# Kernel tuning notes

Hardware: AMD Instinct MI355X
Metric: run time of the kernel (lower is better)

The kernel has to match this reference:

```python
import jax, jax.numpy as jnp
import numpy as np

B = 2048      # number of binary mixtures
NPM = 30      # atoms per molecule
N = B * NPM   # total nodes per side
EPM = 120     # directed edges per molecule
IN_DIM = 74
H = 128
NC = 2


def setup_inputs() -> dict:
    key = jax.random.key(0)
    ks = jax.random.split(key, 24)
    rng = np.random.default_rng(0)
    off = np.repeat(np.arange(B, dtype=np.int64) * NPM, EPM)
    mk_idx = lambda: jnp.asarray((rng.integers(0, NPM, B * EPM) + off).astype(np.int32))

    def lin(k, fi, fo):
        return (jax.random.normal(k, (fi, fo), jnp.float32) / np.sqrt(fi)).astype(jnp.float32)

    inp = {
        'h1': jax.random.normal(ks[0], (N, IN_DIM), jnp.float32),
        'h2': jax.random.normal(ks[1], (N, IN_DIM), jnp.float32),
        'solv1_x': jax.random.uniform(ks[2], (B,), jnp.float32),
        'inter_hb': jax.random.uniform(ks[3], (B,), jnp.float32),
        'intra_hb1': jax.random.uniform(ks[4], (B,), jnp.float32),
        'intra_hb2': jax.random.uniform(ks[5], (B,), jnp.float32),
        'Wg1': lin(ks[6], IN_DIM, H), 'bg1': jnp.zeros((H,), jnp.float32),
        'Wg2': lin(ks[7], H, H), 'bg2': jnp.zeros((H,), jnp.float32),
        'Wp': lin(ks[8], H, H), 'bp': jnp.zeros((H,), jnp.float32),
        'We1': lin(ks[9], 1, 32), 'be1': jnp.zeros((32,), jnp.float32),
        'We2': lin(ks[10], 32, H * H), 'be2': jnp.zeros((H * H,), jnp.float32),
        'bnn': jnp.zeros((H,), jnp.float32),
        'Wih': lin(ks[11], H, 3 * H), 'bih': jnp.zeros((3 * H,), jnp.float32),
        'Whh': lin(ks[12], H, 3 * H), 'bhh': jnp.zeros((3 * H,), jnp.float32),
        'Wcl1': lin(ks[13], 2 * H, H), 'bcl1': jnp.zeros((H,), jnp.float32),
        'Wcl2': lin(ks[14], H, H), 'bcl2': jnp.zeros((H,), jnp.float32),
        'Wcl3': lin(ks[15], H, NC), 'bcl3': jnp.zeros((NC,), jnp.float32),
        'src1': mk_idx(), 'dst1': mk_idx(), 'src2': mk_idx(), 'dst2': mk_idx(),
    }
    return inp


def _graphconv(x, src, dst, W, b, n):
    # DGL GraphConv, norm='both': D_in^{-1/2} A D_out^{-1/2} X W + b
    ones = jnp.ones(src.shape[0], x.dtype)
    d_out = jnp.maximum(jax.ops.segment_sum(ones, src, num_segments=n), 1.0)
    d_in = jnp.maximum(jax.ops.segment_sum(ones, dst, num_segments=n), 1.0)
    m = (x * jax.lax.rsqrt(d_out)[:, None])[src]
    agg = jax.ops.segment_sum(m, dst, num_segments=n)
    return (agg * jax.lax.rsqrt(d_in)[:, None]) @ W + b


def _gru_step(x, h, Wih, bih, Whh, bhh):
    gi = x @ Wih + bih
    gh = h @ Whh + bhh
    ir, iz, ih = jnp.split(gi, 3, axis=-1)
    hr, hz, hn = jnp.split(gh, 3, axis=-1)
    r = jax.nn.sigmoid(ir + hr)
    z = jax.nn.sigmoid(iz + hz)
    n = jnp.tanh(ih + r * hn)
    return (1.0 - z) * n + z * h


def _forward(h1, h2, solv1_x, inter_hb, intra_hb1, intra_hb2,
             Wg1, bg1, Wg2, bg2, Wp, bp, We1, be1, We2, be2, bnn,
             Wih, bih, Whh, bhh, Wcl1, bcl1, Wcl2, bcl2, Wcl3, bcl3,
             src1, dst1, src2, dst2):
    # shared GraphConv layers on both molecule graphs
    t1 = jax.nn.relu(_graphconv(h1, src1, dst1, Wg1, bg1, N))
    t1 = jax.nn.relu(_graphconv(t1, src1, dst1, Wg2, bg2, N))
    t2 = jax.nn.relu(_graphconv(h2, src2, dst2, Wg1, bg1, N))
    t2 = jax.nn.relu(_graphconv(t2, src2, dst2, Wg2, bg2, N))
    # dgl.mean_nodes: per-molecule mean (uniform NPM nodes per molecule)
    hg1 = t1.reshape(B, NPM, H).mean(axis=1) * solv1_x[:, None]
    hg2 = t2.reshape(B, NPM, H).mean(axis=1) * (1.0 - solv1_x)[:, None]
    x = jnp.concatenate([hg1, hg2], axis=0)  # (2B, H)

    # empty_solvsys: inter edges i<->i+B (both dirs) then self-loops
    ar = jnp.arange(B, dtype=jnp.int32)
    ss = jnp.concatenate([ar, ar + B, ar, ar + B])
    sd = jnp.concatenate([ar + B, ar, ar, ar + B])
    ef = jnp.concatenate([inter_hb, inter_hb, intra_hb1, intra_hb2])[:, None]  # (4B,1)

    # MPNNconv: project, NNConv(sum) + GRU, 1 message-passing step
    x = jax.nn.relu(x @ Wp + bp)
    hstate = x
    for _ in range(1):
        w = (jax.nn.relu(ef @ We1 + be1) @ We2 + be2).reshape(-1, H, H)  # (4B,H,H)
        msg = jnp.einsum('ed,edf->ef', x[ss], w)
        agg = jax.ops.segment_sum(msg, sd, num_segments=2 * B) + bnn
        x = _gru_step(jax.nn.relu(agg), hstate, Wih, bih, Whh, bhh)
        hstate = x

    hg = jnp.concatenate([x[:B], x[B:]], axis=1)  # (B, 2H)
    o = jax.nn.relu(hg @ Wcl1 + bcl1)
    o = jax.nn.relu(o @ Wcl2 + bcl2)
    return o @ Wcl3 + bcl3


def reference(h1, h2, solv1_x, inter_hb, intra_hb1, intra_hb2,
              Wg1, bg1, Wg2, bg2, Wp, bp, We1, be1, We2, be2, bnn,
              Wih, bih, Whh, bhh, Wcl1, bcl1, Wcl2, bcl2, Wcl3, bcl3,
              src1, dst1, src2, dst2):
    return _forward(h1, h2, solv1_x, inter_hb, intra_hb1, intra_hb2,
                    Wg1, bg1, Wg2, bg2, Wp, bp, We1, be1, We2, be2, bnn,
                    Wih, bih, Whh, bhh, Wcl1, bcl1, Wcl2, bcl2, Wcl3, bcl3,
                    src1, dst1, src2, dst2)
```

## Files before the change

kernel.cpp:

```cpp
#include <hip/hip_runtime.h>
#include <hip/hip_bf16.h>
#include <math.h>

#define B2    2048
#define NPM   30
#define EPM   120

typedef __attribute__((ext_vector_type(8))) short short8;
typedef __attribute__((ext_vector_type(4))) float f32x4;

__device__ __forceinline__ ushort f2bf(float x) {
  unsigned u = __float_as_uint(x);
  return (ushort)((u + 0x7FFFu + ((u >> 16) & 1u)) >> 16);
}
__device__ __forceinline__ float bf2f(ushort h) {
  return __uint_as_float(((unsigned)h) << 16);
}

__device__ __forceinline__ int swz128(int r, int kb) { return r * 128 + (kb ^ ((r & 7) << 4)); }
__device__ __forceinline__ int swz256(int r, int kb) { return r * 256 + (kb ^ ((r & 15) << 4)); }

struct PrepDescs {
  const float* W[9];
  ushort* hi[9];
  ushort* lo[9];
  int Kreal[9], Kpad[9], N[9];
  int blk0[10];
};

__global__ __launch_bounds__(256) void prep_all_kernel(PrepDescs d)
{
  int b = blockIdx.x;
  int di = 0;
  #pragma unroll
  for (int j = 1; j < 9; ++j) if (b >= d.blk0[j]) di = j;
  if (di == 8) {
    int idx = (b - d.blk0[8]) * 256 + threadIdx.x;
    const float* We2 = d.W[8];
    ushort* hi = d.hi[8];
    ushort* lo = d.lo[8];
    int k = idx >> 11;
    int rem = idx & 2047;
    int n = rem >> 4;
    int d8 = (rem & 15) << 3;
    #pragma unroll
    for (int j = 0; j < 8; ++j) {
      int dd = d8 + j;
      float x = We2[k * 16384 + dd * 128 + n];
      ushort h = f2bf(x);
      hi[k * 16384 + n * 128 + dd] = h;
      lo[k * 16384 + n * 128 + dd] = f2bf(x - bf2f(h));
    }
    return;
  }
  int idx = (b - d.blk0[di]) * 256 + threadIdx.x;
  int Kp8 = d.Kpad[di] >> 3;
  int tot = d.N[di] * Kp8;
  if (idx >= tot) return;
  int n = idx / Kp8;
  int k8 = (idx - n * Kp8) << 3;
  const float* W = d.W[di];
  ushort* hi = d.hi[di];
  ushort* lo = d.lo[di];
  int Kreal = d.Kreal[di], Kpad = d.Kpad[di], N = d.N[di];
  #pragma unroll
  for (int j = 0; j < 8; ++j) {
    int k = k8 + j;
    float x = (k < Kreal) ? W[(long)k * N + n] : 0.f;
    ushort h = f2bf(x);
    hi[(long)n * Kpad + k] = h;
    lo[(long)n * Kpad + k] = f2bf(x - bf2f(h));
  }
}

__global__ __launch_bounds__(256, 4) void grufuse_kernel(
    const float* __restrict__ aggA, const float* __restrict__ aggB,
    const float* __restrict__ zb, const float* __restrict__ bnn,
    const float* __restrict__ xp,
    const ushort* __restrict__ Wihh, const ushort* __restrict__ Wihl,
    const float* __restrict__ bih,
    const ushort* __restrict__ Whhh, const ushort* __restrict__ Whhl,
    const float* __restrict__ bhh,
    float* __restrict__ xnew)
{
  __shared__ __align__(16) char A1h[8192], A1l[8192];
  __shared__ __align__(16) char A2h[8192], A2l[8192];
  __shared__ __align__(16) char Bh[4096], Bl[4096];
  const int tid = threadIdx.x;
  const int w = tid >> 6, l = tid & 63;
  const int rt = blockIdx.x >> 2;
  const int qt = blockIdx.x & 3;
  const long rowBase = (long)rt * 32;
  const int rw = w & 1;
  const int cs = w >> 1;
  const int ar = rw * 16 + (l & 15);
  const int crow = rw * 16 + ((l >> 4) << 2);

  #pragma unroll
  for (int q = 0; q < 4; ++q) {
    int t = tid + 256 * q;
    int r = t >> 5, k4 = (t & 31) << 2;
    long gr = rowBase + r;
    long i = (gr < B2) ? gr : (gr - B2);
    float4 za = *(const float4*)&zb[i * 128 + k4];
    float4 zc = *(const float4*)&zb[(i + B2) * 128 + k4];
    float4 bn = *(const float4*)&bnn[k4];
    const float* ap = (gr < B2) ? &aggA[i * 128 + k4] : &aggB[i * 128 + k4];
    float4 ag = *(const float4*)ap;
    float4 xv;
    xv.x = fmaxf(ag.x + za.x + zc.x + bn.x, 0.f);
    xv.y = fmaxf(ag.y + za.y + zc.y + bn.y, 0.f);
    xv.z = fmaxf(ag.z + za.z + zc.z + bn.z, 0.f);
    xv.w = fmaxf(ag.w + za.w + zc.w + bn.w, 0.f);
    ushort4 h4, l4;
    h4.x = f2bf(xv.x); l4.x = f2bf(xv.x - bf2f(h4.x));
    h4.y = f2bf(xv.y); l4.y = f2bf(xv.y - bf2f(h4.y));
    h4.z = f2bf(xv.z); l4.z = f2bf(xv.z - bf2f(h4.z));
    h4.w = f2bf(xv.w); l4.w = f2bf(xv.w - bf2f(h4.w));
    *(ushort4*)(A1h + swz256(r, k4 * 2)) = h4;
    *(ushort4*)(A1l + swz256(r, k4 * 2)) = l4;
    float4 pv = *(const float4*)&xp[gr * 128 + k4];
    h4.x = f2bf(pv.x); l4.x = f2bf(pv.x - bf2f(h4.x));
    h4.y = f2bf(pv.y); l4.y = f2bf(pv.y - bf2f(h4.y));
    h4.z = f2bf(pv.z); l4.z = f2bf(pv.z - bf2f(h4.z));
    h4.w = f2bf(pv.w); l4.w = f2bf(pv.w - bf2f(h4.w));
    *(ushort4*)(A2h + swz256(r, k4 * 2)) = h4;
    *(ushort4*)(A2l + swz256(r, k4 * 2)) = l4;
  }
  __syncthreads();

  f32x4 rg = (f32x4){0,0,0,0}, zg = (f32x4){0,0,0,0};

  for (int gate = 0; gate < 3; ++gate) {
    f32x4 gi = (f32x4){0,0,0,0}, gh = (f32x4){0,0,0,0};
    for (int src = 0; src < 2; ++src) {
      const ushort* Wh = src ? Whhh : Wihh;
      const ushort* Wl = src ? Whhl : Wihl;
      const char* Ah = src ? A2h : A1h;
      const char* Al = src ? A2l : A1l;
      for (int k0 = 0; k0 < 128; k0 += 64) {
        __syncthreads();
        {
          int n = tid >> 3, k8 = (tid & 7) << 3;
          long wrow = (long)(gate * 128 + qt * 32 + n);
          *(uint4*)(Bh + swz128(n, k8 * 2)) = *(const uint4*)&Wh[wrow * 128 + k0 + k8];
          *(uint4*)(Bl + swz128(n, k8 * 2)) = *(const uint4*)&Wl[wrow * 128 + k0 + k8];
        }
        __syncthreads();
        f32x4 a = (src == 0) ? gi : gh;
        #pragma unroll
        for (int ks = 0; ks < 2; ++ks) {
          const int ko = ks * 32 + (l >> 4) * 8;
          short8 ah  = *(const short8*)(Ah + swz256(ar, (k0 + ko) * 2));
          short8 al8 = *(const short8*)(Al + swz256(ar, (k0 + ko) * 2));
          const int c = cs * 16 + (l & 15);
          short8 bh  = *(const short8*)(Bh + swz128(c, ko * 2));
          short8 bl8 = *(const short8*)(Bl + swz128(c, ko * 2));
          a = __builtin_amdgcn_mfma_f32_16x16x32_bf16(al8, bh, a, 0, 0, 0);
          a = __builtin_amdgcn_mfma_f32_16x16x32_bf16(ah, bl8, a, 0, 0, 0);
          a = __builtin_amdgcn_mfma_f32_16x16x32_bf16(ah, bh, a, 0, 0, 0);
        }
        if (src == 0) gi = a; else gh = a;
      }
    }
    int cg = qt * 32 + cs * 16 + (l & 15);
    float bi = bih[gate * 128 + cg], bh2 = bhh[gate * 128 + cg];
    #pragma unroll
    for (int i = 0; i < 4; ++i) {
      float a = gi[i] + bi;
      float b = gh[i] + bh2;
      if (gate == 0) {
        rg[i] = 1.f / (1.f + expf(-(a + b)));
      } else if (gate == 1) {
        zg[i] = 1.f / (1.f + expf(-(a + b)));
      } else {
        float ng = tanhf(a + rg[i] * b);
        long row = rowBase + crow + i;
        float h = xp[row * 128 + cg];
        xnew[row * 128 + cg] = (1.f - zg[i]) * ng + zg[i] * h;
      }
    }
  }
}

__global__ __launch_bounds__(256, 3) void xpzb_kernel(
    const float* __restrict__ xcat,
    const ushort* __restrict__ Wph, const ushort* __restrict__ Wpl,
    const float* __restrict__ bp,
    const ushort* __restrict__ be2h, const ushort* __restrict__ be2l,
    float* __restrict__ xp, float* __restrict__ zb,
    float* __restrict__ aggZero)
{
  __shared__ __align__(16) char AhB[8192], AlB[8192];
  __shared__ __align__(16) char BhB[16384], BlB[16384];
  const int tid = threadIdx.x;
  const int w = tid >> 6, l = tid & 63;
  const long rowBase = (long)blockIdx.x * 32;
  const int rw = w & 1, ch2 = w >> 1;
  const int ar = rw * 16 + (l & 15);
  const int crow = rw * 16 + ((l >> 4) << 2);

  {
    const float4 z4 = make_float4(0.f, 0.f, 0.f, 0.f);
    long base = (long)(blockIdx.x * 256 + tid) * 4;
    long stride = (long)gridDim.x * 256 * 4;
    for (long t = base; t < 524288; t += stride)
      *(float4*)&aggZero[t] = z4;
  }

  #pragma unroll
  for (int q = 0; q < 4; ++q) {
    int t = tid + 256 * q;
    int r = t >> 5, k4 = (t & 31) << 2;
    float4 v = *(const float4*)&xcat[(rowBase + r) * 128 + k4];
    ushort4 h4, l4;
    h4.x = f2bf(v.x); l4.x = f2bf(v.x - bf2f(h4.x));
    h4.y = f2bf(v.y); l4.y = f2bf(v.y - bf2f(h4.y));
    h4.z = f2bf(v.z); l4.z = f2bf(v.z - bf2f(h4.z));
    h4.w = f2bf(v.w); l4.w = f2bf(v.w - bf2f(h4.w));
    *(ushort4*)(AhB + swz256(r, k4 * 2)) = h4;
    *(ushort4*)(AlB + swz256(r, k4 * 2)) = l4;
  }
  __syncthreads();

  f32x4 acc[4];
  #pragma unroll
  for (int fc = 0; fc < 4; ++fc) acc[fc] = (f32x4){0.f, 0.f, 0.f, 0.f};
  for (int k0 = 0; k0 < 128; k0 += 64) {
    #pragma unroll
    for (int q = 0; q < 4; ++q) {
      int lin = tid + 256 * q;
      int n = lin >> 3, k8 = (lin & 7) << 3;
      *(uint4*)(BhB + swz128(n, k8 * 2)) = *(const uint4*)&Wph[n * 128 + k0 + k8];
      *(uint4*)(BlB + swz128(n, k8 * 2)) = *(const uint4*)&Wpl[n * 128 + k0 + k8];
    }
    __syncthreads();
    #pragma unroll
    for (int ks = 0; ks < 2; ++ks) {
      const int ko = ks * 32 + (l >> 4) * 8;
      short8 ah  = *(const short8*)(AhB + swz256(ar, (k0 + ko) * 2));
      short8 al8 = *(const short8*)(AlB + swz256(ar, (k0 + ko) * 2));
      #pragma unroll
      for (int fc = 0; fc < 4; ++fc) {
        const int c = ch2 * 64 + fc * 16 + (l & 15);
        short8 bh  = *(const short8*)(BhB + swz128(c, ko * 2));
        short8 bl8 = *(const short8*)(BlB + swz128(c, ko * 2));
        acc[fc] = __builtin_amdgcn_mfma_f32_16x16x32_bf16(al8, bh, acc[fc], 0, 0, 0);
        acc[fc] = __builtin_amdgcn_mfma_f32_16x16x32_bf16(ah, bl8, acc[fc], 0, 0, 0);
        acc[fc] = __builtin_amdgcn_mfma_f32_16x16x32_bf16(ah, bh, acc[fc], 0, 0, 0);
      }
    }
    __syncthreads();
  }

  #pragma unroll
  for (int fc = 0; fc < 4; ++fc) {
    int col = ch2 * 64 + fc * 16 + (l & 15);
    float bv = bp[col];
    #pragma unroll
    for (int i = 0; i < 4; ++i) {
      int lr = crow + i;
      float v = fmaxf(acc[fc][i] + bv, 0.f);
      xp[(rowBase + lr) * 128 + col] = v;
      ushort h = f2bf(v);
      *(ushort*)(AhB + swz256(lr, col * 2)) = h;
      *(ushort*)(AlB + swz256(lr, col * 2)) = f2bf(v - bf2f(h));
    }
  }

  #pragma unroll
  for (int fc = 0; fc < 4; ++fc) acc[fc] = (f32x4){0.f, 0.f, 0.f, 0.f};
  for (int k0 = 0; k0 < 128; k0 += 64) {
    __syncthreads();
    #pragma unroll
    for (int q = 0; q < 4; ++q) {
      int lin = tid + 256 * q;
      int n = lin >> 3, k8 = (lin & 7) << 3;
      *(uint4*)(BhB + swz128(n, k8 * 2)) = *(const uint4*)&be2h[n * 128 + k0 + k8];
      *(uint4*)(BlB + swz128(n, k8 * 2)) = *(const uint4*)&be2l[n * 128 + k0 + k8];
    }
    __syncthreads();
    #pragma unroll
    for (int ks = 0; ks < 2; ++ks) {
      const int ko = ks * 32 + (l >> 4) * 8;
      short8 ah  = *(const short8*)(AhB + swz256(ar, (k0 + ko) * 2));
      short8 al8 = *(const short8*)(AlB + swz256(ar, (k0 + ko) * 2));
      #pragma unroll
      for (int fc = 0; fc < 4; ++fc) {
        const int c = ch2 * 64 + fc * 16 + (l & 15);
        short8 bh  = *(const short8*)(BhB + swz128(c, ko * 2));
        short8 bl8 = *(const short8*)(BlB + swz128(c, ko * 2));
        acc[fc] = __builtin_amdgcn_mfma_f32_16x16x32_bf16(al8, bh, acc[fc], 0, 0, 0);
        acc[fc] = __builtin_amdgcn_mfma_f32_16x16x32_bf16(ah, bl8, acc[fc], 0, 0, 0);
        acc[fc] = __builtin_amdgcn_mfma_f32_16x16x32_bf16(ah, bh, acc[fc], 0, 0, 0);
      }
    }
  }
  #pragma unroll
  for (int fc = 0; fc < 4; ++fc) {
    int col = ch2 * 64 + fc * 16 + (l & 15);
    #pragma unroll
    for (int i = 0; i < 4; ++i) {
      int lr = crow + i;
      zb[(rowBase + lr) * 128 + col] = acc[fc][i];
    }
  }
}

__global__ __launch_bounds__(256, 2) void cls_kernel(
    const float* __restrict__ xnew,
    const ushort* __restrict__ W1h, const ushort* __restrict__ W1l,
    const float* __restrict__ b1,
    const ushort* __restrict__ W2h, const ushort* __restrict__ W2l,
    const float* __restrict__ b2,
    const float* __restrict__ Wcl3, const float* __restrict__ bcl3,
    float* __restrict__ out)
{
  __shared__ __align__(16) char O1h[8192], O1l[8192];
  __shared__ __align__(16) char AhB[4096], AlB[4096];
  __shared__ __align__(16) char BhB[16384], BlB[16384];
  __shared__ float redP[64];
  const int tid = threadIdx.x;
  const int w = tid >> 6, l = tid & 63;
  const long rowBase = (long)blockIdx.x * 32;
  const int rw = w & 1, ch2 = w >> 1;
  const int ar = rw * 16 + (l & 15);
  const int crow = rw * 16 + ((l >> 4) << 2);
  if (tid < 64) redP[tid] = 0.f;

  f32x4 acc[4];
  #pragma unroll
  for (int fc = 0; fc < 4; ++fc) acc[fc] = (f32x4){0.f, 0.f, 0.f, 0.f};
  for (int k0 = 0; k0 < 256; k0 += 64) {
    const float* Ab = (k0 < 128) ? xnew : (xnew + (long)B2 * 128);
    const int kc = k0 & 127;
    #pragma unroll
    for (int q = 0; q < 2; ++q) {
      int lin = tid + 256 * q;
      int r = lin >> 4, k4 = (lin & 15) << 2;
      float4 v = *(const float4*)&Ab[(rowBase + r) * 128 + kc + k4];
      ushort4 h4, l4;
      h4.x = f2bf(v.x); l4.x = f2bf(v.x - bf2f(h4.x));
      h4.y = f2bf(v.y); l4.y = f2bf(v.y - bf2f(h4.y));
      h4.z = f2bf(v.z); l4.z = f2bf(v.z - bf2f(h4.z));
      h4.w = f2bf(v.w); l4.w = f2bf(v.w - bf2f(h4.w));
      *(ushort4*)(AhB + swz128(r, k4 * 2)) = h4;
      *(ushort4*)(AlB + swz128(r, k4 * 2)) = l4;
    }
    #pragma unroll
    for (int q = 0; q < 4; ++q) {
      int lin = tid + 256 * q;
      int n = lin >> 3, k8 = (lin & 7) << 3;
      *(uint4*)(BhB + swz128(n, k8 * 2)) = *(const uint4*)&W1h[(long)n * 256 + k0 + k8];
      *(uint4*)(BlB + swz128(n, k8 * 2)) = *(const uint4*)&W1l[(long)n * 256 + k0 + k8];
    }
    __syncthreads();
    #pragma unroll
    for (int ks = 0; ks < 2; ++ks) {
      const int ko = ks * 32 + (l >> 4) * 8;
      short8 ah  = *(const short8*)(AhB + swz128(ar, ko * 2));
      short8 al8 = *(const short8*)(AlB + swz128(ar, ko * 2));
      #pragma unroll
      for (int fc = 0; fc < 4; ++fc) {
        const int c = ch2 * 64 + fc * 16 + (l & 15);
        short8 bh  = *(const short8*)(BhB + swz128(c, ko * 2));
        short8 bl8 = *(const short8*)(BlB + swz128(c, ko * 2));
        acc[fc] = __builtin_amdgcn_mfma_f32_16x16x32_bf16(al8, bh, acc[fc], 0, 0, 0);
        acc[fc] = __builtin_amdgcn_mfma_f32_16x16x32_bf16(ah, bl8, acc[fc], 0, 0, 0);
        acc[fc] = __builtin_amdgcn_mfma_f32_16x16x32_bf16(ah, bh, acc[fc], 0, 0, 0);
      }
    }
    __syncthreads();
  }
  #pragma unroll
  for (int fc = 0; fc < 4; ++fc) {
    int col = ch2 * 64 + fc * 16 + (l & 15);
    float bv = b1[col];
    #pragma unroll
    for (int i = 0; i < 4; ++i) {
      int lr = crow + i;
      float v = fmaxf(acc[fc][i] + bv, 0.f);
      ushort h = f2bf(v);
      *(ushort*)(O1h + swz256(lr, col * 2)) = h;
      *(ushort*)(O1l + swz256(lr, col * 2)) = f2bf(v - bf2f(h));
    }
  }

  #pragma unroll
  for (int fc = 0; fc < 4; ++fc) acc[fc] = (f32x4){0.f, 0.f, 0.f, 0.f};
  for (int k0 = 0; k0 < 128; k0 += 64) {
    __syncthreads();
    #pragma unroll
    for (int q = 0; q < 4; ++q) {
      int lin = tid + 256 * q;
      int n = lin >> 3, k8 = (lin & 7) << 3;
      *(uint4*)(BhB + swz128(n, k8 * 2)) = *(const uint4*)&W2h[n * 128 + k0 + k8];
      *(uint4*)(BlB + swz128(n, k8 * 2)) = *(const uint4*)&W2l[n * 128 + k0 + k8];
    }
    __syncthreads();
    #pragma unroll
    for (int ks = 0; ks < 2; ++ks) {
      const int ko = ks * 32 + (l >> 4) * 8;
      short8 ah  = *(const short8*)(O1h + swz256(ar, (k0 + ko) * 2));
      short8 al8 = *(const short8*)(O1l + swz256(ar, (k0 + ko) * 2));
      #pragma unroll
      for (int fc = 0; fc < 4; ++fc) {
        const int c = ch2 * 64 + fc * 16 + (l & 15);
        short8 bh  = *(const short8*)(BhB + swz128(c, ko * 2));
        short8 bl8 = *(const short8*)(BlB + swz128(c, ko * 2));
        acc[fc] = __builtin_amdgcn_mfma_f32_16x16x32_bf16(al8, bh, acc[fc], 0, 0, 0);
        acc[fc] = __builtin_amdgcn_mfma_f32_16x16x32_bf16(ah, bl8, acc[fc], 0, 0, 0);
        acc[fc] = __builtin_amdgcn_mfma_f32_16x16x32_bf16(ah, bh, acc[fc], 0, 0, 0);
      }
    }
  }

  float p0[4] = {0.f, 0.f, 0.f, 0.f}, p1[4] = {0.f, 0.f, 0.f, 0.f};
  #pragma unroll
  for (int fc = 0; fc < 4; ++fc) {
    int col = ch2 * 64 + fc * 16 + (l & 15);
    float bv = b2[col];
    float w0 = Wcl3[col * 2], w1 = Wcl3[col * 2 + 1];
    #pragma unroll
    for (int i = 0; i < 4; ++i) {
      float v = fmaxf(acc[fc][i] + bv, 0.f);
      p0[i] = fmaf(v, w0, p0[i]);
      p1[i] = fmaf(v, w1, p1[i]);
    }
  }
  __syncthreads();
  #pragma unroll
  for (int i = 0; i < 4; ++i) {
    #pragma unroll
    for (int m = 1; m < 16; m <<= 1) {
      p0[i] += __shfl_xor(p0[i], m);
      p1[i] += __shfl_xor(p1[i], m);
    }
    if ((l & 15) == 0) {
      atomicAdd(&redP[(crow + i) * 2 + 0], p0[i]);
      atomicAdd(&redP[(crow + i) * 2 + 1], p1[i]);
    }
  }
  __syncthreads();
  if (tid < 64) {
    int row = tid >> 1, c = tid & 1;
    out[(rowBase + row) * 2 + c] = redP[row * 2 + c] + bcl3[c];
  }
}

__global__ __launch_bounds__(256, 1) void zfold_mfma_kernel(
    const float* __restrict__ xp,
    const ushort* __restrict__ We2h, const ushort* __restrict__ We2l,
    const float* __restrict__ interhb, const float* __restrict__ ia1,
    const float* __restrict__ ia2, const float* __restrict__ We1,
    const float* __restrict__ be1,
    float* __restrict__ aggA, float* __restrict__ aggB)
{
  __shared__ __align__(16) ushort Ah[2][64 * 72], Al[2][64 * 72];
  __shared__ __align__(16) ushort Bh[128 * 72], Bl[128 * 72];
  __shared__ float accAs[32 * 128], accBs[32 * 128];
  __shared__ float ehs[3][32][8];
  const int tid = threadIdx.x;
  const int w = tid >> 6, l = tid & 63;
  const int rg = blockIdx.x >> 2, kq = blockIdx.x & 3;
  const int i0 = rg * 32;

  for (int t = tid; t < 2048; t += 256) {
    int r = t >> 5, k4 = (t & 31) << 2;
    int gr = (r < 32) ? (i0 + r) : (B2 + i0 + r - 32);
    float4 v = *(const float4*)&xp[(long)gr * 128 + k4];
    int ch = k4 >> 6, ko = k4 & 63;
    ushort4 h4, l4;
    h4.x = f2bf(v.x); l4.x = f2bf(v.x - bf2f(h4.x));
    h4.y = f2bf(v.y); l4.y = f2bf(v.y - bf2f(h4.y));
    h4.z = f2bf(v.z); l4.z = f2bf(v.z - bf2f(h4.z));
    h4.w = f2bf(v.w); l4.w = f2bf(v.w - bf2f(h4.w));
    *(ushort4*)&Ah[ch][r * 72 + ko] = h4;
    *(ushort4*)&Al[ch][r * 72 + ko] = l4;
  }
  for (int t = tid; t < 768; t += 256) {
    int grp = t >> 8, rem = t & 255;
    int mm = rem >> 3, kk = rem & 7;
    int k = kq * 8 + kk;
    float u = (grp == 0) ? interhb[i0 + mm] : (grp == 1) ? ia1[i0 + mm] : ia2[i0 + mm];
    ehs[grp][mm][kk] = fmaxf(fmaf(u, We1[k], be1[k]), 0.f);
  }
  for (int t = tid; t < 4096; t += 256) { accAs[t] = 0.f; accBs[t] = 0.f; }

  float foldA[8][4] = {{0.f}}, foldB[8][4] = {{0.f}};
  const int ar = w * 16 + (l & 15);

  for (int kk = 0; kk < 8; ++kk) {
    const int k = kq * 8 + kk;
    f32x4 acc[8];
    #pragma unroll
    for (int fc = 0; fc < 8; ++fc) acc[fc] = (f32x4){0.f, 0.f, 0.f, 0.f};
    for (int ch = 0; ch < 2; ++ch) {
      __syncthreads();
      #pragma unroll
      for (int q = 0; q < 4; ++q) {
        int lin = tid + 256 * q;
        int n = lin >> 3, k8 = (lin & 7) << 3;
        *(uint4*)&Bh[n * 72 + k8] = *(const uint4*)&We2h[k * 16384 + n * 128 + ch * 64 + k8];
        *(uint4*)&Bl[n * 72 + k8] = *(const uint4*)&We2l[k * 16384 + n * 128 + ch * 64 + k8];
      }
      __syncthreads();
      #pragma unroll
      for (int ks = 0; ks < 2; ++ks) {
        const int ko = ks * 32 + (l >> 4) * 8;
        short8 ah  = *(const short8*)&Ah[ch][ar * 72 + ko];
        short8 al8 = *(const short8*)&Al[ch][ar * 72 + ko];
        #pragma unroll
        for (int fc = 0; fc < 8; ++fc) {
          const int c = fc * 16 + (l & 15);
          short8 bh  = *(const short8*)&Bh[c * 72 + ko];
          short8 bl8 = *(const short8*)&Bl[c * 72 + ko];
          acc[fc] = __builtin_amdgcn_mfma_f32_16x16x32_bf16(al8, bh, acc[fc], 0, 0, 0);
          acc[fc] = __builtin_amdgcn_mfma_f32_16x16x32_bf16(ah, bl8, acc[fc], 0, 0, 0);
          acc[fc] = __builtin_amdgcn_mfma_f32_16x16x32_bf16(ah, bh, acc[fc], 0, 0, 0);
        }
      }
    }
    #pragma unroll
    for (int i = 0; i < 4; ++i) {
      int lr = w * 16 + ((l >> 4) << 2) + i;
      int m = lr & 31, up = lr >> 5;
      float eA = up ? ehs[0][m][kk] : ehs[1][m][kk];
      float eB = up ? ehs[2][m][kk] : ehs[0][m][kk];
      #pragma unroll
      for (int fc = 0; fc < 8; ++fc) {
        foldA[fc][i] = fmaf(eA, acc[fc][i], foldA[fc][i]);
        foldB[fc][i] = fmaf(eB, acc[fc][i], foldB[fc][i]);
      }
    }
  }
  #pragma unroll
  for (int i = 0; i < 4; ++i) {
    int lr = w * 16 + ((l >> 4) << 2) + i;
    int m = lr & 31;
    #pragma unroll
    for (int fc = 0; fc < 8; ++fc) {
      int c = fc * 16 + (l & 15);
      atomicAdd(&accAs[m * 128 + c], foldA[fc][i]);
      atomicAdd(&accBs[m * 128 + c], foldB[fc][i]);
    }
  }
  __syncthreads();
  for (int t = tid; t < 4096; t += 256) {
    int mm = t >> 7, c = t & 127;
    atomicAdd(&aggA[(long)(i0 + mm) * 128 + c], accAs[t]);
    atomicAdd(&aggB[(long)(i0 + mm) * 128 + c], accBs[t]);
  }
}

__global__ __launch_bounds__(512, 4) void gconv_kernel(
    const float* __restrict__ h1, const float* __restrict__ h2,
    const int* __restrict__ src1, const int* __restrict__ dst1,
    const int* __restrict__ src2, const int* __restrict__ dst2,
    const float* __restrict__ bg1,
    const ushort* __restrict__ W1h, const ushort* __restrict__ W1l,
    const ushort* __restrict__ W2h, const ushort* __restrict__ W2l,
    const float* __restrict__ bias2, const float* __restrict__ s1x,
    float* __restrict__ xcat)
{
  __shared__ __align__(16) char pool[75264];
  char* AhB = pool;
  char* AlB = pool + 16384;
  char* BhB = pool + 32768;
  char* BlB = pool + 49152;
  char* A2h = pool;
  char* A2l = pool + 8192;
  char* Byh = pool + 32768;
  char* Byl = pool + 49152;
  float* cs = (float*)(pool + 65536);
  float* cntS = (float*)(pool + 66560);
  float* rsIS = (float*)(pool + 74752);
  float* rsOS = (float*)(pool + 75008);

  const int tid = threadIdx.x;
  const int p = blockIdx.x;
  const int g = p >> 10;
  const int mloc = (p & 1023) * 2;
  const float* hsrc = g ? h2 : h1;
  if (tid < 256) cs[tid] = 0.f;
  for (int t = tid; t < 2176; t += 512) cntS[t] = 0.f;

  const int w8 = tid >> 6, l = tid & 63;
  const int rw = w8 & 3;
  const int ch2 = w8 >> 2;
  const int ar = rw * 16 + (l & 15);
  const int crow = rw * 16 + ((l >> 4) << 2);

  #pragma unroll
  for (int q = 0; q < 4; ++q) {
    int lin = tid + 512 * q;
    int r = lin >> 5, k4 = (lin & 31) << 2;
    float4 v = make_float4(0.f, 0.f, 0.f, 0.f);
    if (r < 60) {
      const float* Ar = &hsrc[(long)(mloc * 30 + r) * 74];
      if (k4 + 4 <= 74) {
        float2 a = *(const float2*)&Ar[k4];
        float2 b = *(const float2*)&Ar[k4 + 2];
        v = make_float4(a.x, a.y, b.x, b.y);
      } else if (k4 + 2 <= 74) {
        float2 a = *(const float2*)&Ar[k4];
        v.x = a.x; v.y = a.y;
      }
    }
    ushort4 h4, l4;
    h4.x = f2bf(v.x); l4.x = f2bf(v.x - bf2f(h4.x));
    h4.y = f2bf(v.y); l4.y = f2bf(v.y - bf2f(h4.y));
    h4.z = f2bf(v.z); l4.z = f2bf(v.z - bf2f(h4.z));
    h4.w = f2bf(v.w); l4.w = f2bf(v.w - bf2f(h4.w));
    *(ushort4*)(AhB + swz256(r, k4 * 2)) = h4;
    *(ushort4*)(AlB + swz256(r, k4 * 2)) = l4;
  }
  __syncthreads();

  f32x4 acc[4];
  #pragma unroll
  for (int fc = 0; fc < 4; ++fc) acc[fc] = (f32x4){0.f, 0.f, 0.f, 0.f};
  for (int k0 = 0; k0 < 128; k0 += 64) {
    if (k0 == 0 && tid < 2 * EPM) {
      int mol = tid / EPM, e = tid - mol * EPM;
      const int* srcp = g ? src2 : src1;
      const int* dstp = g ? dst2 : dst1;
      int m = mloc + mol;
      int s = srcp[m * EPM + e] - m * NPM;
      int d = dstp[m * EPM + e] - m * NPM;
      atomicAdd(&cntS[mol * 990 + d * 33 + s], 1.0f);
    }
    #pragma unroll
    for (int q = 0; q < 2; ++q) {
      int lin = tid + 512 * q;
      int n = lin >> 3, k8 = (lin & 7) << 3;
      *(uint4*)(BhB + swz128(n, k8 * 2)) = *(const uint4*)&W1h[n * 128 + k0 + k8];
      *(uint4*)(BlB + swz128(n, k8 * 2)) = *(const uint4*)&W1l[n * 128 + k0 + k8];
    }
    __syncthreads();
    #pragma unroll
    for (int ks = 0; ks < 2; ++ks) {
      const int ko = ks * 32 + (l >> 4) * 8;
      short8 ah  = *(const short8*)(AhB + swz256(ar, (k0 + ko) * 2));
      short8 al8 = *(const short8*)(AlB + swz256(ar, (k0 + ko) * 2));
      #pragma unroll
      for (int fc = 0; fc < 4; ++fc) {
        const int c = ch2 * 64 + fc * 16 + (l & 15);
        short8 bh  = *(const short8*)(BhB + swz128(c, ko * 2));
        short8 bl8 = *(const short8*)(BlB + swz128(c, ko * 2));
        acc[fc] = __builtin_amdgcn_mfma_f32_16x16x32_bf16(al8, bh, acc[fc], 0, 0, 0);
        acc[fc] = __builtin_amdgcn_mfma_f32_16x16x32_bf16(ah, bl8, acc[fc], 0, 0, 0);
        acc[fc] = __builtin_amdgcn_mfma_f32_16x16x32_bf16(ah, bh, acc[fc], 0, 0, 0);
      }
    }
    if (k0 == 0) {
      if (tid < 60) {
        int mol = tid / 30, r = tid - mol * 30;
        float s = 0.f;
        for (int k = 0; k < 30; ++k) s += cntS[mol * 990 + r * 33 + k];
        rsIS[mol * 32 + r] = rsqrtf(fmaxf(s, 1.f));
      } else if (tid >= 64 && tid < 124) {
        int t2 = tid - 64;
        int mol = t2 / 30, sc = t2 - mol * 30;
        float s = 0.f;
        for (int d = 0; d < 30; ++d) s += cntS[mol * 990 + d * 33 + sc];
        rsOS[mol * 32 + sc] = rsqrtf(fmaxf(s, 1.f));
      }
    }
    __syncthreads();
  }

  #pragma unroll
  for (int fc = 0; fc < 4; ++fc) {
    int n = ch2 * 64 + fc * 16 + (l & 15);
    ushort4 h4, l4;
    h4.x = f2bf(acc[fc][0]); l4.x = f2bf(acc[fc][0] - bf2f(h4.x));
    h4.y = f2bf(acc[fc][1]); l4.y = f2bf(acc[fc][1] - bf2f(h4.y));
    h4.z = f2bf(acc[fc][2]); l4.z = f2bf(acc[fc][2] - bf2f(h4.z));
    h4.w = f2bf(acc[fc][3]); l4.w = f2bf(acc[fc][3] - bf2f(h4.w));
    *(ushort4*)(Byh + swz128(n, crow * 2)) = h4;
    *(ushort4*)(Byl + swz128(n, crow * 2)) = l4;
  }
  for (int t = tid; t < 4096; t += 512) {
    int row = t >> 6, k = t & 63;
    float v = 0.f;
    if (row < 30) {
      if (k < 30) v = cntS[row * 33 + k] * rsIS[row] * rsOS[k];
    } else if (row < 60) {
      if (k >= 30 && k < 60)
        v = cntS[990 + (row - 30) * 33 + (k - 30)] * rsIS[32 + row - 30] * rsOS[32 + k - 30];
    }
    ushort h = f2bf(v);
    *(ushort*)(A2h + swz128(row, k * 2)) = h;
    *(ushort*)(A2l + swz128(row, k * 2)) = f2bf(v - bf2f(h));
  }
  __syncthreads();

  f32x4 acc2[4];
  #pragma unroll
  for (int fc = 0; fc < 4; ++fc) acc2[fc] = (f32x4){0.f, 0.f, 0.f, 0.f};
  #pragma unroll
  for (int ks = 0; ks < 2; ++ks) {
    const int ko = ks * 32 + (l >> 4) * 8;
    short8 ah  = *(const short8*)(A2h + swz128(ar, ko * 2));
    short8 al8 = *(const short8*)(A2l + swz128(ar, ko * 2));
    #pragma unroll
    for (int fc = 0; fc < 4; ++fc) {
      const int c = ch2 * 64 + fc * 16 + (l & 15);
      short8 bh  = *(const short8*)(Byh + swz128(c, ko * 2));
      short8 bl8 = *(const short8*)(Byl + swz128(c, ko * 2));
      acc2[fc] = __builtin_amdgcn_mfma_f32_16x16x32_bf16(al8, bh, acc2[fc], 0, 0, 0);
      acc2[fc] = __builtin_amdgcn_mfma_f32_16x16x32_bf16(ah, bl8, acc2[fc], 0, 0, 0);
      acc2[fc] = __builtin_amdgcn_mfma_f32_16x16x32_bf16(ah, bh, acc2[fc], 0, 0, 0);
    }
  }
  __syncthreads();

  #pragma unroll
  for (int fc = 0; fc < 4; ++fc) {
    int n = ch2 * 64 + fc * 16 + (l & 15);
    float bv = bg1[n];
    float t0 = fmaxf(acc2[fc][0] + bv, 0.f);
    float t1v = fmaxf(acc2[fc][1] + bv, 0.f);
    float t2v = fmaxf(acc2[fc][2] + bv, 0.f);
    float t3 = fmaxf(acc2[fc][3] + bv, 0.f);
    ushort4 h4, l4;
    h4.x = f2bf(t0); l4.x = f2bf(t0 - bf2f(h4.x));
    h4.y = f2bf(t1v); l4.y = f2bf(t1v - bf2f(h4.y));
    h4.z = f2bf(t2v); l4.z = f2bf(t2v - bf2f(h4.z));
    h4.w = f2bf(t3); l4.w = f2bf(t3 - bf2f(h4.w));
    *(ushort4*)(Byh + swz128(n, crow * 2)) = h4;
    *(ushort4*)(Byl + swz128(n, crow * 2)) = l4;
  }
  __syncthreads();

  #pragma unroll
  for (int fc = 0; fc < 4; ++fc) acc2[fc] = (f32x4){0.f, 0.f, 0.f, 0.f};
  #pragma unroll
  for (int ks = 0; ks < 2; ++ks) {
    const int ko = ks * 32 + (l >> 4) * 8;
    short8 ah  = *(const short8*)(A2h + swz128(ar, ko * 2));
    short8 al8 = *(const short8*)(A2l + swz128(ar, ko * 2));
    #pragma unroll
    for (int fc = 0; fc < 4; ++fc) {
      const int c = ch2 * 64 + fc * 16 + (l & 15);
      short8 bh  = *(const short8*)(Byh + swz128(c, ko * 2));
      short8 bl8 = *(const short8*)(Byl + swz128(c, ko * 2));
      acc2[fc] = __builtin_amdgcn_mfma_f32_16x16x32_bf16(al8, bh, acc2[fc], 0, 0, 0);
      acc2[fc] = __builtin_amdgcn_mfma_f32_16x16x32_bf16(ah, bl8, acc2[fc], 0, 0, 0);
      acc2[fc] = __builtin_amdgcn_mfma_f32_16x16x32_bf16(ah, bh, acc2[fc], 0, 0, 0);
    }
  }
  __syncthreads();

  #pragma unroll
  for (int fc = 0; fc < 4; ++fc) {
    int n = ch2 * 64 + fc * 16 + (l & 15);
    #pragma unroll
    for (int i = 0; i < 4; ++i) {
      int r = crow + i;
      ushort h = f2bf(acc2[fc][i]);
      *(ushort*)(AhB + swz256(r, n * 2)) = h;
      *(ushort*)(AlB + swz256(r, n * 2)) = f2bf(acc2[fc][i] - bf2f(h));
    }
  }

  #pragma unroll
  for (int fc = 0; fc < 4; ++fc) acc[fc] = (f32x4){0.f, 0.f, 0.f, 0.f};
  for (int k0 = 0; k0 < 128; k0 += 64) {
    __syncthreads();
    #pragma unroll
    for (int q = 0; q < 2; ++q) {
      int lin = tid + 512 * q;
      int n = lin >> 3, k8 = (lin & 7) << 3;
      *(uint4*)(BhB + swz128(n, k8 * 2)) = *(const uint4*)&W2h[n * 128 + k0 + k8];
      *(uint4*)(BlB + swz128(n, k8 * 2)) = *(const uint4*)&W2l[n * 128 + k0 + k8];
    }
    __syncthreads();
    #pragma unroll
    for (int ks = 0; ks < 2; ++ks) {
      const int ko = ks * 32 + (l >> 4) * 8;
      short8 ah  = *(const short8*)(AhB + swz256(ar, (k0 + ko) * 2));
      short8 al8 = *(const short8*)(AlB + swz256(ar, (k0 + ko) * 2));
      #pragma unroll
      for (int fc = 0; fc < 4; ++fc) {
        const int c = ch2 * 64 + fc * 16 + (l & 15);
        short8 bh  = *(const short8*)(BhB + swz128(c, ko * 2));
        short8 bl8 = *(const short8*)(BlB + swz128(c, ko * 2));
        acc[fc] = __builtin_amdgcn_mfma_f32_16x16x32_bf16(al8, bh, acc[fc], 0, 0, 0);
        acc[fc] = __builtin_amdgcn_mfma_f32_16x16x32_bf16(ah, bl8, acc[fc], 0, 0, 0);
        acc[fc] = __builtin_amdgcn_mfma_f32_16x16x32_bf16(ah, bh, acc[fc], 0, 0, 0);
      }
    }
  }
  __syncthreads();

  #pragma unroll
  for (int fc = 0; fc < 4; ++fc) {
    int col = ch2 * 64 + fc * 16 + (l & 15);
    float bv = bias2[col];
    float s0 = 0.f, s1 = 0.f;
    #pragma unroll
    for (int i = 0; i < 4; ++i) {
      int lr = crow + i;
      if (lr < 60) {
        float v = fmaxf(acc[fc][i] + bv, 0.f);
        if (lr < NPM) s0 += v; else s1 += v;
      }
    }
    s0 += __shfl_down(s0, 32); s0 += __shfl_down(s0, 16);
    s1 += __shfl_down(s1, 32); s1 += __shfl_down(s1, 16);
    if ((l >> 4) == 0) {
      atomicAdd(&cs[col], s0);
      atomicAdd(&cs[128 + col], s1);
    }
  }
  __syncthreads();
  if (tid < 256) {
    int moll = tid >> 7, c = tid & 127;
    int gm = p * 2 + moll;
    int gg = gm >> 11, mm = gm & 2047;
    float sf = gg ? (1.f - s1x[mm]) : s1x[mm];
    xcat[(long)gm * 128 + c] = cs[moll * 128 + c] * (1.f / 30.f) * sf;
  }
}

extern "C" void kernel_launch(void* const* d_in, const int* in_sizes, int n_in,
                              void* d_out, int out_size, void* d_ws, size_t ws_size,
                              hipStream_t stream)
{
  const float* h1   = (const float*)d_in[0];
  const float* h2   = (const float*)d_in[1];
  const float* s1x  = (const float*)d_in[2];
  const float* ihb  = (const float*)d_in[3];
  const float* ia1  = (const float*)d_in[4];
  const float* ia2  = (const float*)d_in[5];
  const float* Wg1  = (const float*)d_in[6];
  const float* bg1  = (const float*)d_in[7];
  const float* Wg2  = (const float*)d_in[8];
  const float* bg2  = (const float*)d_in[9];
  const float* Wp   = (const float*)d_in[10];
  const float* bp   = (const float*)d_in[11];
  const float* We1  = (const float*)d_in[12];
  const float* be1  = (const float*)d_in[13];
  const float* We2  = (const float*)d_in[14];
  const float* be2  = (const float*)d_in[15];
  const float* bnn  = (const float*)d_in[16];
  const float* Wih  = (const float*)d_in[17];
  const float* bih  = (const float*)d_in[18];
  const float* Whh  = (const float*)d_in[19];
  const float* bhh  = (const float*)d_in[20];
  const float* Wcl1 = (const float*)d_in[21];
  const float* bcl1 = (const float*)d_in[22];
  const float* Wcl2 = (const float*)d_in[23];
  const float* bcl2 = (const float*)d_in[24];
  const float* Wcl3 = (const float*)d_in[25];
  const float* bcl3 = (const float*)d_in[26];
  const int*   src1 = (const int*)d_in[27];
  const int*   dst1 = (const int*)d_in[28];
  const int*   src2 = (const int*)d_in[29];
  const int*   dst2 = (const int*)d_in[30];
  float* out = (float*)d_out;
  float* ws  = (float*)d_ws;

  float* dwn  = ws + 35389440;

  float* xcat = dwn;
  float* xp   = dwn + 524288;
  float* zb   = dwn + 1048576;
  float* aggA = dwn + 1572864;
  float* aggB = dwn + 1835008;
  float* xnew = dwn + 2097152;

  ushort* wt     = (ushort*)(dwn + 6815744);
  ushort* WpTh   = wt;               ushort* WpTl   = wt + 16384;
  ushort* be2Th  = wt + 32768;       ushort* be2Tl  = wt + 49152;
  ushort* WihTh  = wt + 65536;       ushort* WihTl  = wt + 114688;
  ushort* WhhTh  = wt + 163840;      ushort* WhhTl  = wt + 212992;
  ushort* Wcl1Th = wt + 262144;      ushort* Wcl1Tl = wt + 294912;
  ushort* Wcl2Th = wt + 327680;      ushort* Wcl2Tl = wt + 344064;
  ushort* Wg1Th  = wt + 360448;      ushort* Wg1Tl  = wt + 376832;
  ushort* Wg2Th  = wt + 393216;      ushort* Wg2Tl  = wt + 409600;
  ushort* We2h   = wt + 425984;      ushort* We2l   = wt + 950272;

  PrepDescs pd;
  const float* Ws_[9]  = {Wp, be2, Wih, Whh, Wcl1, Wcl2, Wg1, Wg2, We2};
  ushort* his[9]       = {WpTh, be2Th, WihTh, WhhTh, Wcl1Th, Wcl2Th, Wg1Th, Wg2Th, We2h};
  ushort* los[9]       = {WpTl, be2Tl, WihTl, WhhTl, Wcl1Tl, Wcl2Tl, Wg1Tl, Wg2Tl, We2l};
  int kr[9]   = {128, 128, 128, 128, 256, 128, 74, 128, 0};
  int kp[9]   = {128, 128, 128, 128, 256, 128, 128, 128, 0};
  int nn[9]   = {128, 128, 384, 384, 128, 128, 128, 128, 0};
  int acc_blk = 0;
  for (int i = 0; i < 8; ++i) {
    pd.W[i] = Ws_[i]; pd.hi[i] = his[i]; pd.lo[i] = los[i];
    pd.Kreal[i] = kr[i]; pd.Kpad[i] = kp[i]; pd.N[i] = nn[i];
    pd.blk0[i] = acc_blk;
    acc_blk += (nn[i] * (kp[i] >> 3) + 255) / 256;
  }
  pd.W[8] = Ws_[8]; pd.hi[8] = his[8]; pd.lo[8] = los[8];
  pd.Kreal[8] = 0; pd.Kpad[8] = 0; pd.N[8] = 0;
  pd.blk0[8] = acc_blk;
  acc_blk += 256;
  pd.blk0[9] = acc_blk;
  prep_all_kernel<<<acc_blk, 256, 0, stream>>>(pd);

  gconv_kernel<<<2048, 512, 0, stream>>>(h1, h2, src1, dst1, src2, dst2,
                                         bg1, Wg1Th, Wg1Tl, Wg2Th, Wg2Tl,
                                         bg2, s1x, xcat);

  xpzb_kernel<<<128, 256, 0, stream>>>(xcat, WpTh, WpTl, bp, be2Th, be2Tl,
                                       xp, zb, aggA);
  zfold_mfma_kernel<<<256, 256, 0, stream>>>(xp, We2h, We2l, ihb, ia1, ia2,
                                             We1, be1, aggA, aggB);
  grufuse_kernel<<<512, 256, 0, stream>>>(aggA, aggB, zb, bnn, xp,
                                          WihTh, WihTl, bih, WhhTh, WhhTl, bhh,
                                          xnew);
  cls_kernel<<<64, 256, 0, stream>>>(xnew, Wcl1Th, Wcl1Tl, bcl1,
                                     Wcl2Th, Wcl2Tl, bcl2, Wcl3, bcl3, out);
}
```

Measured before the change: 164.9 us.

## Process one molecule per gconv block instead of two to cut padding and LDS

Restructures gconv_kernel so each block handles a single 30-atom molecule (32-row tile) instead of two molecules packed into a 64-row tile. Grid doubles to 4096 blocks, LDS shrinks from about 75KB to about 54KB, launch bounds rise to 6 blocks per CU, and the adjacency GEMM shrinks from K=64 to K=32 with a single k-step. This removes the wasted block-diagonal zero work and aims for higher occupancy. In exchange, the W1/W2 weight tiles are now loaded into LDS twice as often overall, and per-block fixed overhead is amortised over half the rows.

After: 169.3 us. 1.03x slower.

```diff
diff --git a/kernel.cpp b/kernel.cpp
--- a/kernel.cpp
+++ b/kernel.cpp
@@ -553,7 +553,7 @@
   }
 }
 
-__global__ __launch_bounds__(512, 4) void gconv_kernel(
+__global__ __launch_bounds__(512, 6) void gconv_kernel(
     const float* __restrict__ h1, const float* __restrict__ h2,
     const int* __restrict__ src1, const int* __restrict__ dst1,
     const int* __restrict__ src2, const int* __restrict__ dst2,
@@ -563,41 +563,41 @@
     const float* __restrict__ bias2, const float* __restrict__ s1x,
     float* __restrict__ xcat)
 {
-  __shared__ __align__(16) char pool[75264];
+  __shared__ __align__(16) char pool[53888];
   char* AhB = pool;
-  char* AlB = pool + 16384;
-  char* BhB = pool + 32768;
-  char* BlB = pool + 49152;
+  char* AlB = pool + 8192;
+  char* BhB = pool + 16384;
+  char* BlB = pool + 32768;
   char* A2h = pool;
-  char* A2l = pool + 8192;
-  char* Byh = pool + 32768;
-  char* Byl = pool + 49152;
-  float* cs = (float*)(pool + 65536);
-  float* cntS = (float*)(pool + 66560);
-  float* rsIS = (float*)(pool + 74752);
-  float* rsOS = (float*)(pool + 75008);
+  char* A2l = pool + 4096;
+  char* Byh = pool + 16384;
+  char* Byl = pool + 32768;
+  float* cs   = (float*)(pool + 49152);
+  float* cntS = (float*)(pool + 49664);
+  float* rsIS = (float*)(pool + 53624);
+  float* rsOS = (float*)(pool + 53752);
 
   const int tid = threadIdx.x;
   const int p = blockIdx.x;
-  const int g = p >> 10;
-  const int mloc = (p & 1023) * 2;
+  const int g = p >> 11;
+  const int m = p & 2047;
   const float* hsrc = g ? h2 : h1;
-  if (tid < 256) cs[tid] = 0.f;
-  for (int t = tid; t < 2176; t += 512) cntS[t] = 0.f;
+  if (tid < 128) cs[tid] = 0.f;
+  for (int t = tid; t < 1054; t += 512) cntS[t] = 0.f;
 
   const int w8 = tid >> 6, l = tid & 63;
-  const int rw = w8 & 3;
-  const int ch2 = w8 >> 2;
+  const int rw = w8 & 1;
+  const int ch4 = w8 >> 1;
   const int ar = rw * 16 + (l & 15);
   const int crow = rw * 16 + ((l >> 4) << 2);
 
   #pragma unroll
-  for (int q = 0; q < 4; ++q) {
+  for (int q = 0; q < 2; ++q) {
     int lin = tid + 512 * q;
     int r = lin >> 5, k4 = (lin & 31) << 2;
     float4 v = make_float4(0.f, 0.f, 0.f, 0.f);
-    if (r < 60) {
-      const float* Ar = &hsrc[(long)(mloc * 30 + r) * 74];
+    if (r < 30) {
+      const float* Ar = &hsrc[(long)(m * 30 + r) * 74];
       if (k4 + 4 <= 74) {
         float2 a = *(const float2*)&Ar[k4];
         float2 b = *(const float2*)&Ar[k4 + 2];
@@ -617,18 +617,16 @@
   }
   __syncthreads();
 
-  f32x4 acc[4];
-  #pragma unroll
-  for (int fc = 0; fc < 4; ++fc) acc[fc] = (f32x4){0.f, 0.f, 0.f, 0.f};
+  f32x4 acc[2];
+  #pragma unroll
+  for (int fc = 0; fc < 2; ++fc) acc[fc] = (f32x4){0.f, 0.f, 0.f, 0.f};
   for (int k0 = 0; k0 < 128; k0 += 64) {
-    if (k0 == 0 && tid < 2 * EPM) {
-      int mol = tid / EPM, e = tid - mol * EPM;
+    if (k0 == 0 && tid < EPM) {
       const int* srcp = g ? src2 : src1;
       const int* dstp = g ? dst2 : dst1;
-      int m = mloc + mol;
-      int s = srcp[m * EPM + e] - m * NPM;
-      int d = dstp[m * EPM + e] - m * NPM;
-      atomicAdd(&cntS[mol * 990 + d * 33 + s], 1.0f);
+      int s = srcp[m * EPM + tid] - m * NPM;
+      int d = dstp[m * EPM + tid] - m * NPM;
+      atomicAdd(&cntS[d * 33 + s], 1.0f);
     }
     #pragma unroll
     for (int q = 0; q < 2; ++q) {
@@ -644,8 +642,8 @@
       short8 ah  = *(const short8*)(AhB + swz256(ar, (k0 + ko) * 2));
       short8 al8 = *(const short8*)(AlB + swz256(ar, (k0 + ko) * 2));
       #pragma unroll
-      for (int fc = 0; fc < 4; ++fc) {
-        const int c = ch2 * 64 + fc * 16 + (l & 15);
+      for (int fc = 0; fc < 2; ++fc) {
+        const int c = ch4 * 32 + fc * 16 + (l & 15);
         short8 bh  = *(const short8*)(BhB + swz128(c, ko * 2));
         short8 bl8 = *(const short8*)(BlB + swz128(c, ko * 2));
         acc[fc] = __builtin_amdgcn_mfma_f32_16x16x32_bf16(al8, bh, acc[fc], 0, 0, 0);
@@ -654,25 +652,23 @@
       }
     }
     if (k0 == 0) {
-      if (tid < 60) {
-        int mol = tid / 30, r = tid - mol * 30;
+      if (tid < 30) {
         float s = 0.f;
-        for (int k = 0; k < 30; ++k) s += cntS[mol * 990 + r * 33 + k];
-        rsIS[mol * 32 + r] = rsqrtf(fmaxf(s, 1.f));
-      } else if (tid >= 64 && tid < 124) {
-        int t2 = tid - 64;
-        int mol = t2 / 30, sc = t2 - mol * 30;
+        for (int k = 0; k < 30; ++k) s += cntS[tid * 33 + k];
+        rsIS[tid] = rsqrtf(fmaxf(s, 1.f));
+      } else if (tid >= 64 && tid < 94) {
+        int sc = tid - 64;
         float s = 0.f;
-        for (int d = 0; d < 30; ++d) s += cntS[mol * 990 + d * 33 + sc];
-        rsOS[mol * 32 + sc] = rsqrtf(fmaxf(s, 1.f));
-      }
-    }
-    __syncthreads();
-  }
-
-  #pragma unroll
-  for (int fc = 0; fc < 4; ++fc) {
-    int n = ch2 * 64 + fc * 16 + (l & 15);
+        for (int d = 0; d < 30; ++d) s += cntS[d * 33 + sc];
+        rsOS[sc] = rsqrtf(fmaxf(s, 1.f));
+      }
+    }
+    __syncthreads();
+  }
+
+  #pragma unroll
+  for (int fc = 0; fc < 2; ++fc) {
+    int n = ch4 * 32 + fc * 16 + (l & 15);
     ushort4 h4, l4;
     h4.x = f2bf(acc[fc][0]); l4.x = f2bf(acc[fc][0] - bf2f(h4.x));
     h4.y = f2bf(acc[fc][1]); l4.y = f2bf(acc[fc][1] - bf2f(h4.y));
@@ -681,32 +677,26 @@
     *(ushort4*)(Byh + swz128(n, crow * 2)) = h4;
     *(ushort4*)(Byl + swz128(n, crow * 2)) = l4;
   }
-  for (int t = tid; t < 4096; t += 512) {
+  for (int t = tid; t < 2048; t += 512) {
     int row = t >> 6, k = t & 63;
-    float v = 0.f;
-    if (row < 30) {
-      if (k < 30) v = cntS[row * 33 + k] * rsIS[row] * rsOS[k];
-    } else if (row < 60) {
-      if (k >= 30 && k < 60)
-        v = cntS[990 + (row - 30) * 33 + (k - 30)] * rsIS[32 + row - 30] * rsOS[32 + k - 30];
-    }
+    float v = (row < 30 && k < 30)
+            ? cntS[row * 33 + k] * rsIS[row] * rsOS[k] : 0.f;
     ushort h = f2bf(v);
     *(ushort*)(A2h + swz128(row, k * 2)) = h;
     *(ushort*)(A2l + swz128(row, k * 2)) = f2bf(v - bf2f(h));
   }
   __syncthreads();
 
-  f32x4 acc2[4];
-  #pragma unroll
-  for (int fc = 0; fc < 4; ++fc) acc2[fc] = (f32x4){0.f, 0.f, 0.f, 0.f};
-  #pragma unroll
-  for (int ks = 0; ks < 2; ++ks) {
-    const int ko = ks * 32 + (l >> 4) * 8;
+  f32x4 acc2[2];
+  #pragma unroll
+  for (int fc = 0; fc < 2; ++fc) acc2[fc] = (f32x4){0.f, 0.f, 0.f, 0.f};
+  {
+    const int ko = (l >> 4) * 8;
     short8 ah  = *(const short8*)(A2h + swz128(ar, ko * 2));
     short8 al8 = *(const short8*)(A2l + swz128(ar, ko * 2));
     #pragma unroll
-    for (int fc = 0; fc < 4; ++fc) {
-      const int c = ch2 * 64 + fc * 16 + (l & 15);
+    for (int fc = 0; fc < 2; ++fc) {
+      const int c = ch4 * 32 + fc * 16 + (l & 15);
       short8 bh  = *(const short8*)(Byh + swz128(c, ko * 2));
       short8 bl8 = *(const short8*)(Byl + swz128(c, ko * 2));
       acc2[fc] = __builtin_amdgcn_mfma_f32_16x16x32_bf16(al8, bh, acc2[fc], 0, 0, 0);
@@ -717,8 +707,8 @@
   __syncthreads();
 
   #pragma unroll
-  for (int fc = 0; fc < 4; ++fc) {
-    int n = ch2 * 64 + fc * 16 + (l & 15);
+  for (int fc = 0; fc < 2; ++fc) {
+    int n = ch4 * 32 + fc * 16 + (l & 15);
     float bv = bg1[n];
     float t0 = fmaxf(acc2[fc][0] + bv, 0.f);
     float t1v = fmaxf(acc2[fc][1] + bv, 0.f);
@@ -735,15 +725,14 @@
   __syncthreads();
 
   #pragma unroll
-  for (int fc = 0; fc < 4; ++fc) acc2[fc] = (f32x4){0.f, 0.f, 0.f, 0.f};
-  #pragma unroll
-  for (int ks = 0; ks < 2; ++ks) {
-    const int ko = ks * 32 + (l >> 4) * 8;
+  for (int fc = 0; fc < 2; ++fc) acc2[fc] = (f32x4){0.f, 0.f, 0.f, 0.f};
+  {
+    const int ko = (l >> 4) * 8;
     short8 ah  = *(const short8*)(A2h + swz128(ar, ko * 2));
     short8 al8 = *(const short8*)(A2l + swz128(ar, ko * 2));
     #pragma unroll
-    for (int fc = 0; fc < 4; ++fc) {
-      const int c = ch2 * 64 + fc * 16 + (l & 15);
+    for (int fc = 0; fc < 2; ++fc) {
+      const int c = ch4 * 32 + fc * 16 + (l & 15);
       short8 bh  = *(const short8*)(Byh + swz128(c, ko * 2));
       short8 bl8 = *(const short8*)(Byl + swz128(c, ko * 2));
       acc2[fc] = __builtin_amdgcn_mfma_f32_16x16x32_bf16(al8, bh, acc2[fc], 0, 0, 0);
@@ -754,8 +743,8 @@
   __syncthreads();
 
   #pragma unroll
-  for (int fc = 0; fc < 4; ++fc) {
-    int n = ch2 * 64 + fc * 16 + (l & 15);
+  for (int fc = 0; fc < 2; ++fc) {
+    int n = ch4 * 32 + fc * 16 + (l & 15);
     #pragma unroll
     for (int i = 0; i < 4; ++i) {
       int r = crow + i;
@@ -766,7 +755,7 @@
   }
 
   #pragma unroll
-  for (int fc = 0; fc < 4; ++fc) acc[fc] = (f32x4){0.f, 0.f, 0.f, 0.f};
+  for (int fc = 0; fc < 2; ++fc) acc[fc] = (f32x4){0.f, 0.f, 0.f, 0.f};
   for (int k0 = 0; k0 < 128; k0 += 64) {
     __syncthreads();
     #pragma unroll
@@ -783,8 +772,8 @@
       short8 ah  = *(const short8*)(AhB + swz256(ar, (k0 + ko) * 2));
       short8 al8 = *(const short8*)(AlB + swz256(ar, (k0 + ko) * 2));
       #pragma unroll
-      for (int fc = 0; fc < 4; ++fc) {
-        const int c = ch2 * 64 + fc * 16 + (l & 15);
+      for (int fc = 0; fc < 2; ++fc) {
+        const int c = ch4 * 32 + fc * 16 + (l & 15);
         short8 bh  = *(const short8*)(BhB + swz128(c, ko * 2));
         short8 bl8 = *(const short8*)(BlB + swz128(c, ko * 2));
         acc[fc] = __builtin_amdgcn_mfma_f32_16x16x32_bf16(al8, bh, acc[fc], 0, 0, 0);
@@ -796,32 +785,22 @@
   __syncthreads();
 
   #pragma unroll
-  for (int fc = 0; fc < 4; ++fc) {
-    int col = ch2 * 64 + fc * 16 + (l & 15);
+  for (int fc = 0; fc < 2; ++fc) {
+    int col = ch4 * 32 + fc * 16 + (l & 15);
     float bv = bias2[col];
-    float s0 = 0.f, s1 = 0.f;
+    float s0 = 0.f;
     #pragma unroll
     for (int i = 0; i < 4; ++i) {
       int lr = crow + i;
-      if (lr < 60) {
-        float v = fmaxf(acc[fc][i] + bv, 0.f);
-        if (lr < NPM) s0 += v; else s1 += v;
-      }
+      if (lr < NPM) s0 += fmaxf(acc[fc][i] + bv, 0.f);
     }
     s0 += __shfl_down(s0, 32); s0 += __shfl_down(s0, 16);
-    s1 += __shfl_down(s1, 32); s1 += __shfl_down(s1, 16);
-    if ((l >> 4) == 0) {
-      atomicAdd(&cs[col], s0);
-      atomicAdd(&cs[128 + col], s1);
-    }
-  }
-  __syncthreads();
-  if (tid < 256) {
-    int moll = tid >> 7, c = tid & 127;
-    int gm = p * 2 + moll;
-    int gg = gm >> 11, mm = gm & 2047;
-    float sf = gg ? (1.f - s1x[mm]) : s1x[mm];
-    xcat[(long)gm * 128 + c] = cs[moll * 128 + c] * (1.f / 30.f) * sf;
+    if ((l >> 4) == 0) atomicAdd(&cs[col], s0);
+  }
+  __syncthreads();
+  if (tid < 128) {
+    float sf = g ? (1.f - s1x[m]) : s1x[m];
+    xcat[(long)p * 128 + tid] = cs[tid] * (1.f / 30.f) * sf;
   }
 }
 
@@ -904,7 +883,7 @@
   pd.blk0[9] = acc_blk;
   prep_all_kernel<<<acc_blk, 256, 0, stream>>>(pd);
 
-  gconv_kernel<<<2048, 512, 0, stream>>>(h1, h2, src1, dst1, src2, dst2,
+  gconv_kernel<<<4096, 512, 0, stream>>>(h1, h2, src1, dst1, src2, dst2,
                                          bg1, Wg1Th, Wg1Tl, Wg2Th, Wg2Tl,
                                          bg2, s1x, xcat);
 
```
